# Kernel tuning notes

Hardware: AMD Instinct MI355X
Metric: run time of the kernel (lower is better)

The kernel has to match this reference:

```python
import jax, jax.numpy as jnp
import numpy as np

N, E, G = 100000, 1600000, 100
NEG_SLOPE = 0.2
EPS = 1e-5


def gatv2_conv(x, src, dst, Wl, Wr, att, bias, concat):
    # PyG GATv2Conv (eval mode, add_self_loops already applied to src/dst).
    # x: [N, F_in]; Wl/Wr: [F_in, H*C]; att: [H, C]; bias: [H*C] or [C].
    H, C = att.shape
    n = x.shape[0]
    xl = (x @ Wl).reshape(n, H, C)  # source-side transform (messages)
    xr = (x @ Wr).reshape(n, H, C)  # target-side transform
    m = jax.nn.leaky_relu(xl[src] + xr[dst], NEG_SLOPE)      # [Etot, H, C]
    e = jnp.einsum('ehc,hc->eh', m, att)                      # [Etot, H]
    # softmax over incoming edges of each destination node (per head)
    emax = jax.ops.segment_max(e, dst, num_segments=n)        # [n, H]
    ex = jnp.exp(e - emax[dst])
    denom = jax.ops.segment_sum(ex, dst, num_segments=n)
    alpha = ex / denom[dst]                                   # [Etot, H]
    out = jax.ops.segment_sum(xl[src] * alpha[..., None], dst, num_segments=n)  # [n, H, C]
    out = out.reshape(n, H * C) if concat else out.mean(axis=1)
    return out + bias


def graph_norm(x, batch, w, b, mean_scale):
    # PyG GraphNorm: per-graph mean/var with learnable mean_scale.
    cnt = jnp.maximum(jax.ops.segment_sum(jnp.ones((x.shape[0], 1), x.dtype), batch, num_segments=G), 1.0)
    mean = jax.ops.segment_sum(x, batch, num_segments=G) / cnt
    xc = x - mean_scale * mean[batch]
    var = jax.ops.segment_sum(xc * xc, batch, num_segments=G) / cnt
    return w * xc / jnp.sqrt(var[batch] + EPS) + b


def global_mean_pool(x, batch):
    cnt = jnp.maximum(jax.ops.segment_sum(jnp.ones((x.shape[0], 1), x.dtype), batch, num_segments=G), 1.0)
    return jax.ops.segment_sum(x, batch, num_segments=G) / cnt


def setup_inputs() -> dict:
    key = jax.random.key(0)
    ks = jax.random.split(key, 16)
    F_in, H, C12, C3 = 64, 4, 16, 32
    s_in = 1.0 / np.sqrt(F_in)
    s_h = 1.0 / np.sqrt(H * C12)
    inp = {
        'x': jax.random.normal(ks[0], (N, F_in), jnp.float32),
        'edge_index': jax.random.randint(ks[1], (2, E), 0, N, jnp.int64),
        'batch': jnp.sort(jax.random.randint(ks[2], (N,), 0, G, jnp.int64)),
        'Wl1': jax.random.normal(ks[3], (F_in, H * C12), jnp.float32) * s_in,
        'Wr1': jax.random.normal(ks[4], (F_in, H * C12), jnp.float32) * s_in,
        'att1': jax.random.normal(ks[5], (H, C12), jnp.float32) * s_in,
        'b1': jnp.zeros((H * C12,), jnp.float32),
        'g1w': jnp.ones((H * C12,), jnp.float32),
        'g1b': jnp.zeros((H * C12,), jnp.float32),
        'g1a': jnp.ones((H * C12,), jnp.float32),
        'Wl2': jax.random.normal(ks[6], (H * C12, H * C12), jnp.float32) * s_h,
        'Wr2': jax.random.normal(ks[7], (H * C12, H * C12), jnp.float32) * s_h,
        'att2': jax.random.normal(ks[8], (H, C12), jnp.float32) * s_h,
        'b2': jnp.zeros((H * C12,), jnp.float32),
        'g2w': jnp.ones((H * C12,), jnp.float32),
        'g2b': jnp.zeros((H * C12,), jnp.float32),
        'g2a': jnp.ones((H * C12,), jnp.float32),
        'Wl3': jax.random.normal(ks[9], (H * C12, H * C3), jnp.float32) * s_h,
        'Wr3': jax.random.normal(ks[10], (H * C12, H * C3), jnp.float32) * s_h,
        'att3': jax.random.normal(ks[11], (H, C3), jnp.float32) * s_h,
        'b3': jnp.zeros((C3,), jnp.float32),
        'g3w': jnp.ones((C3,), jnp.float32),
        'g3b': jnp.zeros((C3,), jnp.float32),
        'g3a': jnp.ones((C3,), jnp.float32),
        'Wlin': jax.random.normal(ks[12], (C3, 2), jnp.float32) * (1.0 / np.sqrt(C3)),
        'blin': jnp.zeros((2,), jnp.float32),
    }
    return inp


def reference(x, edge_index, batch, Wl1, Wr1, att1, b1, g1w, g1b, g1a,
              Wl2, Wr2, att2, b2, g2w, g2b, g2a,
              Wl3, Wr3, att3, b3, g3w, g3b, g3a, Wlin, blin):
    # add self-loops (GATv2Conv default)
    loops = jnp.arange(N, dtype=edge_index.dtype)
    src = jnp.concatenate([edge_index[0], loops])
    dst = jnp.concatenate([edge_index[1], loops])
    h = jax.nn.relu(graph_norm(gatv2_conv(x, src, dst, Wl1, Wr1, att1, b1, True), batch, g1w, g1b, g1a))
    h = jax.nn.relu(graph_norm(gatv2_conv(h, src, dst, Wl2, Wr2, att2, b2, True), batch, g2w, g2b, g2a))
    h = jax.nn.relu(graph_norm(gatv2_conv(h, src, dst, Wl3, Wr3, att3, b3, False), batch, g3w, g3b, g3a))
    pooled = global_mean_pool(h, batch)  # [G, h3]
    return pooled @ Wlin + blin          # [G, 2]
```

## Files before the change

kernel.cpp:

```cpp
#include <hip/hip_runtime.h>
#include <hip/hip_bf16.h>

#define LEAKY 0.2f
#define EPS_GN 1e-5f
#define PSH 9

typedef unsigned int uint;
typedef __attribute__((ext_vector_type(8))) short bf16x8;
typedef __attribute__((ext_vector_type(4))) float f32x4;


__device__ inline float4 bf4(uint lo, uint hi) {
    union { uint u; float f; } a, b, c, d;
    a.u = lo << 16; b.u = lo & 0xFFFF0000u;
    c.u = hi << 16; d.u = hi & 0xFFFF0000u;
    return make_float4(a.f, b.f, c.f, d.f);
}

__device__ inline uint pack_bf2(float lo, float hi) {
    union { float f; uint u; } x, y; x.f = lo; y.f = hi;
    uint ra = x.u + 0x7FFFu + ((x.u >> 16) & 1u);
    uint rb = y.u + 0x7FFFu + ((y.u >> 16) & 1u);
    return (ra >> 16) | (rb & 0xFFFF0000u);
}

__device__ inline unsigned short pack_bf1(float v) {
    union { float f; uint u; } q; q.f = v;
    return (unsigned short)((q.u + 0x7FFFu + ((q.u >> 16) & 1u)) >> 16);
}


__global__ void setup_kernel(float* __restrict__ stats, int statN,
                             const float* __restrict__ Wl1, const float* __restrict__ Wr1,
                             const float* __restrict__ Wl2, const float* __restrict__ Wr2,
                             const float* __restrict__ Wl3, const float* __restrict__ Wr3,
                             unsigned short* __restrict__ wt1, unsigned short* __restrict__ wt2,
                             unsigned short* __restrict__ wt3,
                             int* __restrict__ pcnt, int* __restrict__ csr_pad,
                             const int* __restrict__ batch, int* __restrict__ goff,
                             int nN, int nG) {
    int idx = blockIdx.x * 256 + threadIdx.x;
    if (idx < statN) { stats[idx] = 0.f; return; }
    idx -= statN;
    if (idx < 8192) {
        int col = idx >> 6, k = idx & 63;
        float v = (col < 64) ? Wl1[k * 64 + col] : Wr1[k * 64 + (col - 64)];
        wt1[col * 64 + k] = pack_bf1(v);
        return;
    }
    idx -= 8192;
    if (idx < 8192) {
        int col = idx >> 6, k = idx & 63;
        float v = (col < 64) ? Wl2[k * 64 + col] : Wr2[k * 64 + (col - 64)];
        wt2[col * 64 + k] = pack_bf1(v);
        return;
    }
    idx -= 8192;
    if (idx < 16384) {
        int col = idx >> 6, k = idx & 63;
        float v = (col < 128) ? Wl3[k * 128 + col] : Wr3[k * 128 + (col - 128)];
        wt3[col * 64 + k] = pack_bf1(v);
        return;
    }
    idx -= 16384;
    if (idx < 256) { pcnt[idx] = 0; return; }
    idx -= 256;
    if (idx < 16) { csr_pad[idx] = 0; return; }
    idx -= 16;
    if (idx <= nG) {
        if (idx == nG) { goff[idx] = nN; return; }
        int lo = 0, hi = nN;
        while (lo < hi) { int mid = (lo + hi) >> 1; if (batch[mid] < idx) lo = mid + 1; else hi = mid; }
        goff[idx] = lo;
    }
}


__global__ void pcount_kernel(const int* __restrict__ dsts, int* __restrict__ pcnt,
                              int E_, int Etot_) {
    __shared__ int h[256];
    int tid = threadIdx.x;
    h[tid] = 0;
    __syncthreads();
    int i0 = blockIdx.x * 2048 + tid;
#pragma unroll
    for (int k = 0; k < 8; ++k) {
        int i = i0 + k * 256;
        if (i < Etot_) {
            int d = (i < E_) ? dsts[i] : (i - E_);
            atomicAdd(&h[d >> PSH], 1);
        }
    }
    __syncthreads();
    if (h[tid] > 0) atomicAdd(&pcnt[tid], h[tid]);
}

__global__ void pscan_kernel(const int* __restrict__ pcnt, int* __restrict__ pstart,
                             int* __restrict__ gcur, int* __restrict__ rowstart, int nN) {
    __shared__ int sd[256];
    int t = threadIdx.x;
    int v = pcnt[t];
    sd[t] = v;
    __syncthreads();
    for (int off = 1; off < 256; off <<= 1) {
        int tmp = (t >= off) ? sd[t - off] : 0;
        __syncthreads();
        sd[t] += tmp;
        __syncthreads();
    }
    int excl = sd[t] - v;
    pstart[t] = excl;
    gcur[t] = excl;
    if (t == 255) {
        pstart[256] = sd[255];
        gcur[256] = sd[255];
        rowstart[nN] = sd[255];
    }
}

__global__ void partA_kernel(const int* __restrict__ srcs, const int* __restrict__ dsts,
                             int* __restrict__ gcur, uint* __restrict__ ebuf,
                             int E_, int Etot_) {
    __shared__ int hist[256], base_s[256], lcur[256];
    int tid = threadIdx.x;
    hist[tid] = 0; lcur[tid] = 0;
    __syncthreads();
    int i0 = blockIdx.x * 2048 + tid;
    uint rec[8]; int pp[8];
#pragma unroll
    for (int k = 0; k < 8; ++k) {
        int i = i0 + k * 256;
        pp[k] = -1;
        if (i < Etot_) {
            int s, d;
            if (i < E_) { s = srcs[i]; d = dsts[i]; } else { s = i - E_; d = s; }
            int p = d >> PSH;
            pp[k] = p;
            rec[k] = (uint)s | ((uint)(d & ((1 << PSH) - 1)) << 17);
            atomicAdd(&hist[p], 1);
        }
    }
    __syncthreads();
    int h = hist[tid];
    if (h > 0) base_s[tid] = atomicAdd(&gcur[tid], h);
    __syncthreads();
#pragma unroll
    for (int k = 0; k < 8; ++k) {
        if (pp[k] >= 0) {
            int pos = base_s[pp[k]] + atomicAdd(&lcur[pp[k]], 1);
            ebuf[pos] = rec[k];
        }
    }
}

__global__ void partB2_kernel(const uint* __restrict__ ebuf, const int* __restrict__ pstart,
                              int* __restrict__ rowstart, int* __restrict__ csr, int nN) {
    __shared__ int cnt[512], ofs[512], ssum[256];
    int t = threadIdx.x;
    cnt[t] = 0; cnt[t + 256] = 0;
    __syncthreads();
    int p = blockIdx.x;
    int lo = pstart[p], hi = pstart[p + 1];
    for (int i = lo + t; i < hi; i += 256)
        atomicAdd(&cnt[ebuf[i] >> 17], 1);
    __syncthreads();
    int a = cnt[2 * t], b = cnt[2 * t + 1];
    ssum[t] = a + b;
    __syncthreads();
    for (int off = 1; off < 256; off <<= 1) {
        int tmp = (t >= off) ? ssum[t - off] : 0;
        __syncthreads();
        ssum[t] += tmp;
        __syncthreads();
    }
    int base = (t > 0) ? ssum[t - 1] : 0;
    ofs[2 * t] = lo + base;
    ofs[2 * t + 1] = lo + base + a;
    __syncthreads();
    int n0 = p << PSH;
#pragma unroll
    for (int j = t; j < 512; j += 256) {
        int n = n0 + j;
        if (n < nN) rowstart[n] = ofs[j];
    }
    __syncthreads();
    for (int i = lo + t; i < hi; i += 256) {
        uint v = ebuf[i];
        int pos = atomicAdd(&ofs[v >> 17], 1);
        csr[pos] = (int)(v & 0x1FFFFu);
    }
}


template <int NCOLS, bool NORM>
__global__ __launch_bounds__(256, 4)
void gemm_mfma_kernel(const float* __restrict__ x, const unsigned short* __restrict__ Wt,
                      unsigned short* __restrict__ xl, unsigned short* __restrict__ xr,
                      int nN, const float* __restrict__ param, const int* __restrict__ batch) {
    constexpr int NT = NCOLS / 16;
    constexpr int OD = NCOLS / 2;
    __shared__ unsigned short Xs[64 * 64];
    __shared__ unsigned short Ws[NCOLS * 64];
    int tid = threadIdx.x;
    int node0 = blockIdx.x * 64;

    {
        int nl = tid >> 2, k0 = (tid & 3) * 16;
        int n = node0 + nl;
        bool v = n < nN;
        int nc = v ? n : 0;
        const float* xrow = x + (size_t)nc * 64 + k0;
        const float* scp = nullptr; const float* shp = nullptr;
        if constexpr (NORM) {
            int g = batch[nc];
            scp = param + (size_t)g * 128 + k0;
            shp = param + (size_t)g * 128 + 64 + k0;
        }
        uint q[8];
#pragma unroll
        for (int j = 0; j < 8; ++j) {
            float a = v ? xrow[j * 2] : 0.f;
            float b = v ? xrow[j * 2 + 1] : 0.f;
            if constexpr (NORM) {
                a = fmaxf(fmaf(scp[j * 2], a, shp[j * 2]), 0.f);
                b = fmaxf(fmaf(scp[j * 2 + 1], b, shp[j * 2 + 1]), 0.f);
            }
            q[j] = pack_bf2(a, b);
        }
        char* base = (char*)Xs + nl * 128;
        uint sw = (uint)(nl & 7) << 4;
        *(uint4*)(base + (((uint)(k0 * 2)) ^ sw))      = make_uint4(q[0], q[1], q[2], q[3]);
        *(uint4*)(base + (((uint)(k0 * 2 + 16)) ^ sw)) = make_uint4(q[4], q[5], q[6], q[7]);
    }
    for (int ch = tid; ch < NCOLS * 8; ch += 256) {
        int col = ch >> 3, sub = ch & 7;
        uint4 q = ((const uint4*)(Wt + col * 64))[sub];
        *(uint4*)((char*)Ws + col * 128 + (((uint)(sub * 16)) ^ ((uint)(col & 7) << 4))) = q;
    }
    __syncthreads();

    int lane = tid & 63;
    int wv = tid >> 6;
    int l15 = lane & 15, quad = lane >> 4;

    bf16x8 xf[2];
    {
        int row = wv * 16 + l15;
        char* base = (char*)Xs + row * 128;
        uint sw = (uint)(row & 7) << 4;
        xf[0] = *(bf16x8*)(base + (((uint)(quad * 16)) ^ sw));
        xf[1] = *(bf16x8*)(base + (((uint)(64 + quad * 16)) ^ sw));
    }
    f32x4 acc[NT];
#pragma unroll
    for (int t = 0; t < NT; ++t) acc[t] = (f32x4){0.f, 0.f, 0.f, 0.f};
#pragma unroll
    for (int t = 0; t < NT; ++t) {
        int col = t * 16 + l15;
        char* base = (char*)Ws + col * 128;
        uint sw = (uint)(col & 7) << 4;
        bf16x8 a0 = *(bf16x8*)(base + (((uint)(quad * 16)) ^ sw));
        bf16x8 a1 = *(bf16x8*)(base + (((uint)(64 + quad * 16)) ^ sw));
        acc[t] = __builtin_amdgcn_mfma_f32_16x16x32_bf16(a0, xf[0], acc[t], 0, 0, 0);
        acc[t] = __builtin_amdgcn_mfma_f32_16x16x32_bf16(a1, xf[1], acc[t], 0, 0, 0);
    }
    int node = node0 + wv * 16 + l15;
    if (node < nN) {
#pragma unroll
        for (int t = 0; t < NT; ++t) {
            int cg = t * 16 + quad * 4;
            unsigned short* outp = (cg < OD) ? xl : xr;
            int ocol = (cg < OD) ? cg : cg - OD;
            uint2 pk;
            pk.x = pack_bf2(acc[t][0], acc[t][1]);
            pk.y = pack_bf2(acc[t][2], acc[t][3]);
            *(uint2*)(outp + (size_t)node * OD + ocol) = pk;
        }
    }
}


__global__ void agg64_kernel(const unsigned short* __restrict__ xl, const unsigned short* __restrict__ xr,
                             const int* __restrict__ rowstart, const int* __restrict__ csr,
                             const float* __restrict__ att, const float* __restrict__ bias,
                             float* __restrict__ out, int nN) {
    int wid = (blockIdx.x * blockDim.x + threadIdx.x) >> 6;
    int lane = threadIdx.x & 63;
    if (wid >= nN) return;
    int c8 = lane & 7;
    int sg = lane >> 3;
    const uint4* xl4 = (const uint4*)xl;
    const float LOG2E = 1.4426950408889634f;
    float4 attA = ((const float4*)att)[c8 * 2];
    float4 attB = ((const float4*)att)[c8 * 2 + 1];
    attA.x *= LOG2E; attA.y *= LOG2E; attA.z *= LOG2E; attA.w *= LOG2E;
    attB.x *= LOG2E; attB.y *= LOG2E; attB.z *= LOG2E; attB.w *= LOG2E;
    uint4 xru = ((const uint4*)xr)[(size_t)wid * 8 + c8];
    float4 xrA = bf4(xru.x, xru.y), xrB = bf4(xru.z, xru.w);
    int rs = rowstart[wid], re = rowstart[wid + 1];
    int nIt = (re - rs + 7) >> 3;
    float den = 0.f;
    float4 accA = make_float4(0.f, 0.f, 0.f, 0.f);
    float4 accB = make_float4(0.f, 0.f, 0.f, 0.f);
    int i = rs + sg;
    int s = csr[i];
    uint4 xv = xl4[(size_t)s * 8 + c8];
    for (int it = 0; it < nIt; ++it) {
        float4 curA = bf4(xv.x, xv.y), curB = bf4(xv.z, xv.w);
        bool vv = i < re;
        i += 8;
        s = csr[i];
        xv = xl4[(size_t)s * 8 + c8];
        float4 mA, mB;
        mA.x = curA.x + xrA.x; mA.y = curA.y + xrA.y;
        mA.z = curA.z + xrA.z; mA.w = curA.w + xrA.w;
        mB.x = curB.x + xrB.x; mB.y = curB.y + xrB.y;
        mB.z = curB.z + xrB.z; mB.w = curB.w + xrB.w;
        mA.x = fmaxf(mA.x, LEAKY * mA.x); mA.y = fmaxf(mA.y, LEAKY * mA.y);
        mA.z = fmaxf(mA.z, LEAKY * mA.z); mA.w = fmaxf(mA.w, LEAKY * mA.w);
        mB.x = fmaxf(mB.x, LEAKY * mB.x); mB.y = fmaxf(mB.y, LEAKY * mB.y);
        mB.z = fmaxf(mB.z, LEAKY * mB.z); mB.w = fmaxf(mB.w, LEAKY * mB.w);
        float p = mA.x * attA.x;
        p = fmaf(mA.y, attA.y, p); p = fmaf(mA.z, attA.z, p); p = fmaf(mA.w, attA.w, p);
        p = fmaf(mB.x, attB.x, p); p = fmaf(mB.y, attB.y, p);
        p = fmaf(mB.z, attB.z, p); p = fmaf(mB.w, attB.w, p);
        p += __shfl_xor(p, 1);
        float w = vv ? exp2f(p) : 0.f;
        den += w;
        accA.x = fmaf(w, curA.x, accA.x); accA.y = fmaf(w, curA.y, accA.y);
        accA.z = fmaf(w, curA.z, accA.z); accA.w = fmaf(w, curA.w, accA.w);
        accB.x = fmaf(w, curB.x, accB.x); accB.y = fmaf(w, curB.y, accB.y);
        accB.z = fmaf(w, curB.z, accB.z); accB.w = fmaf(w, curB.w, accB.w);
    }
#pragma unroll
    for (int off = 8; off <= 32; off <<= 1) {
        den    += __shfl_xor(den, off);
        accA.x += __shfl_xor(accA.x, off); accA.y += __shfl_xor(accA.y, off);
        accA.z += __shfl_xor(accA.z, off); accA.w += __shfl_xor(accA.w, off);
        accB.x += __shfl_xor(accB.x, off); accB.y += __shfl_xor(accB.y, off);
        accB.z += __shfl_xor(accB.z, off); accB.w += __shfl_xor(accB.w, off);
    }
    if (lane < 8) {
        float4 bvA = ((const float4*)bias)[c8 * 2];
        float4 bvB = ((const float4*)bias)[c8 * 2 + 1];
        float inv = 1.f / den;
        float4 rA, rB;
        rA.x = fmaf(accA.x, inv, bvA.x); rA.y = fmaf(accA.y, inv, bvA.y);
        rA.z = fmaf(accA.z, inv, bvA.z); rA.w = fmaf(accA.w, inv, bvA.w);
        rB.x = fmaf(accB.x, inv, bvB.x); rB.y = fmaf(accB.y, inv, bvB.y);
        rB.z = fmaf(accB.z, inv, bvB.z); rB.w = fmaf(accB.w, inv, bvB.w);
        ((float4*)out)[(size_t)wid * 16 + c8 * 2]     = rA;
        ((float4*)out)[(size_t)wid * 16 + c8 * 2 + 1] = rB;
    }
}


__global__ void agg128_mean_kernel(const unsigned short* __restrict__ xl, const unsigned short* __restrict__ xr,
                                   const int* __restrict__ rowstart, const int* __restrict__ csr,
                                   const float* __restrict__ att, const float* __restrict__ bias,
                                   float* __restrict__ out, int nN) {
    int wid = (blockIdx.x * blockDim.x + threadIdx.x) >> 6;
    int lane = threadIdx.x & 63;
    if (wid >= nN) return;
    int c8 = lane & 15;
    int sg = lane >> 4;
    const uint4* xl4 = (const uint4*)xl;
    const float LOG2E = 1.4426950408889634f;
    float4 attA = ((const float4*)att)[c8 * 2];
    float4 attB = ((const float4*)att)[c8 * 2 + 1];
    attA.x *= LOG2E; attA.y *= LOG2E; attA.z *= LOG2E; attA.w *= LOG2E;
    attB.x *= LOG2E; attB.y *= LOG2E; attB.z *= LOG2E; attB.w *= LOG2E;
    uint4 xru = ((const uint4*)xr)[(size_t)wid * 16 + c8];
    float4 xrA = bf4(xru.x, xru.y), xrB = bf4(xru.z, xru.w);
    int rs = rowstart[wid], re = rowstart[wid + 1];
    int nIt = (re - rs + 3) >> 2;
    float den = 0.f;
    float4 accA = make_float4(0.f, 0.f, 0.f, 0.f);
    float4 accB = make_float4(0.f, 0.f, 0.f, 0.f);
    int i = rs + sg;
    int s = csr[i];
    uint4 xv = xl4[(size_t)s * 16 + c8];
    for (int it = 0; it < nIt; ++it) {
        float4 curA = bf4(xv.x, xv.y), curB = bf4(xv.z, xv.w);
        bool vv = i < re;
        i += 4;
        s = csr[i];
        xv = xl4[(size_t)s * 16 + c8];
        float4 mA, mB;
        mA.x = curA.x + xrA.x; mA.y = curA.y + xrA.y;
        mA.z = curA.z + xrA.z; mA.w = curA.w + xrA.w;
        mB.x = curB.x + xrB.x; mB.y = curB.y + xrB.y;
        mB.z = curB.z + xrB.z; mB.w = curB.w + xrB.w;
        mA.x = fmaxf(mA.x, LEAKY * mA.x); mA.y = fmaxf(mA.y, LEAKY * mA.y);
        mA.z = fmaxf(mA.z, LEAKY * mA.z); mA.w = fmaxf(mA.w, LEAKY * mA.w);
        mB.x = fmaxf(mB.x, LEAKY * mB.x); mB.y = fmaxf(mB.y, LEAKY * mB.y);
        mB.z = fmaxf(mB.z, LEAKY * mB.z); mB.w = fmaxf(mB.w, LEAKY * mB.w);
        float p = mA.x * attA.x;
        p = fmaf(mA.y, attA.y, p); p = fmaf(mA.z, attA.z, p); p = fmaf(mA.w, attA.w, p);
        p = fmaf(mB.x, attB.x, p); p = fmaf(mB.y, attB.y, p);
        p = fmaf(mB.z, attB.z, p); p = fmaf(mB.w, attB.w, p);
        p += __shfl_xor(p, 1);
        p += __shfl_xor(p, 2);
        float w = vv ? exp2f(p) : 0.f;
        den += w;
        accA.x = fmaf(w, curA.x, accA.x); accA.y = fmaf(w, curA.y, accA.y);
        accA.z = fmaf(w, curA.z, accA.z); accA.w = fmaf(w, curA.w, accA.w);
        accB.x = fmaf(w, curB.x, accB.x); accB.y = fmaf(w, curB.y, accB.y);
        accB.z = fmaf(w, curB.z, accB.z); accB.w = fmaf(w, curB.w, accB.w);
    }
#pragma unroll
    for (int off = 16; off <= 32; off <<= 1) {
        den    += __shfl_xor(den, off);
        accA.x += __shfl_xor(accA.x, off); accA.y += __shfl_xor(accA.y, off);
        accA.z += __shfl_xor(accA.z, off); accA.w += __shfl_xor(accA.w, off);
        accB.x += __shfl_xor(accB.x, off); accB.y += __shfl_xor(accB.y, off);
        accB.z += __shfl_xor(accB.z, off); accB.w += __shfl_xor(accB.w, off);
    }
    float inv = 1.f / den;
    float4 rA, rB;
    rA.x = accA.x * inv; rA.y = accA.y * inv; rA.z = accA.z * inv; rA.w = accA.w * inv;
    rB.x = accB.x * inv; rB.y = accB.y * inv; rB.z = accB.z * inv; rB.w = accB.w * inv;
#pragma unroll
    for (int off = 4; off <= 8; off <<= 1) {
        rA.x += __shfl_xor(rA.x, off); rA.y += __shfl_xor(rA.y, off);
        rA.z += __shfl_xor(rA.z, off); rA.w += __shfl_xor(rA.w, off);
        rB.x += __shfl_xor(rB.x, off); rB.y += __shfl_xor(rB.y, off);
        rB.z += __shfl_xor(rB.z, off); rB.w += __shfl_xor(rB.w, off);
    }
    if (lane < 4) {
        float4 bvA = ((const float4*)bias)[lane * 2];
        float4 bvB = ((const float4*)bias)[lane * 2 + 1];
        float4 oA, oB;
        oA.x = fmaf(rA.x, 0.25f, bvA.x); oA.y = fmaf(rA.y, 0.25f, bvA.y);
        oA.z = fmaf(rA.z, 0.25f, bvA.z); oA.w = fmaf(rA.w, 0.25f, bvA.w);
        oB.x = fmaf(rB.x, 0.25f, bvB.x); oB.y = fmaf(rB.y, 0.25f, bvB.y);
        oB.z = fmaf(rB.z, 0.25f, bvB.z); oB.w = fmaf(rB.w, 0.25f, bvB.w);
        ((float4*)out)[(size_t)wid * 8 + lane * 2]     = oA;
        ((float4*)out)[(size_t)wid * 8 + lane * 2 + 1] = oB;
    }
}


template <int D>
__global__ void gnorm_stats_kernel(const float* __restrict__ in, const int* __restrict__ goff,
                                   float* __restrict__ stats, int SPLIT) {
    int g = blockIdx.x / SPLIT, part = blockIdx.x % SPLIT;
    int start = goff[g], end = goff[g + 1];
    constexpr int RPB = 256 / D;
    int tid = threadIdx.x;
    int c = tid % D, sub = tid / D;
    float s1 = 0.f, s2 = 0.f;
    for (int n = start + part * RPB + sub; n < end; n += SPLIT * RPB) {
        float v = in[(size_t)n * D + c];
        s1 += v; s2 += v * v;
    }
    __shared__ float l1[256], l2[256];
    l1[tid] = s1; l2[tid] = s2;
    __syncthreads();
    if (tid < D) {
        for (int s = 1; s < RPB; ++s) { s1 += l1[s * D + tid]; s2 += l2[s * D + tid]; }
        atomicAdd(&stats[(size_t)g * 2 * D + tid], s1);
        atomicAdd(&stats[(size_t)g * 2 * D + D + tid], s2);
    }
}

template <int D>
__global__ void gnorm_finalize_kernel(const float* __restrict__ stats, const int* __restrict__ goff,
                                      const float* __restrict__ w, const float* __restrict__ b,
                                      const float* __restrict__ a, float* __restrict__ param) {
    int g = blockIdx.x, c = threadIdx.x;
    if (c >= D) return;
    int cn = goff[g + 1] - goff[g];
    float cnt = (float)(cn > 1 ? cn : 1);
    float S1 = stats[(size_t)g * 2 * D + c], S2 = stats[(size_t)g * 2 * D + D + c];
    float mu = S1 / cnt;
    float am = a[c] * mu;
    float var = S2 / cnt - 2.f * am * mu + am * am;
    float sc = w[c] * rsqrtf(var + EPS_GN);
    param[(size_t)g * 2 * D + c] = sc;
    param[(size_t)g * 2 * D + D + c] = b[c] - sc * am;
}


__global__ void pool3_kernel(const float* __restrict__ in, const int* __restrict__ goff,
                             const float* __restrict__ param, float* __restrict__ pooled, int SPLIT) {
    int g = blockIdx.x / SPLIT, part = blockIdx.x % SPLIT;
    int start = goff[g], end = goff[g + 1];
    int tid = threadIdx.x;
    int c = tid & 31, sub = tid >> 5;
    float sc = param[(size_t)g * 64 + c], sh = param[(size_t)g * 64 + 32 + c];
    float s = 0.f;
    for (int n = start + part * 8 + sub; n < end; n += SPLIT * 8)
        s += fmaxf(fmaf(sc, in[(size_t)n * 32 + c], sh), 0.f);
    __shared__ float l[256];
    l[tid] = s;
    __syncthreads();
    if (tid < 32) {
        for (int q = 1; q < 8; ++q) s += l[q * 32 + tid];
        atomicAdd(&pooled[(size_t)g * 32 + tid], s);
    }
}

__global__ void lin_kernel(const float* __restrict__ pooled, const int* __restrict__ goff,
                           const float* __restrict__ Wlin, const float* __restrict__ blin,
                           float* __restrict__ out, int nG) {
    int idx = blockIdx.x * blockDim.x + threadIdx.x;
    if (idx >= nG * 2) return;
    int g = idx >> 1, o = idx & 1;
    int cn = goff[g + 1] - goff[g];
    float inv = 1.f / (float)(cn > 1 ? cn : 1);
    float acc = blin[o];
    for (int c = 0; c < 32; ++c) acc = fmaf(pooled[(size_t)g * 32 + c] * inv, Wlin[c * 2 + o], acc);
    out[idx] = acc;
}


extern "C" void kernel_launch(void* const* d_in, const int* in_sizes, int n_in,
                              void* d_out, int out_size, void* d_ws, size_t ws_size,
                              hipStream_t stream) {
    const float* x    = (const float*)d_in[0];
    const int*  eidx  = (const int*)d_in[1];
    const int*  batch = (const int*)d_in[2];
    const float* Wl1 = (const float*)d_in[3];
    const float* Wr1 = (const float*)d_in[4];
    const float* att1 = (const float*)d_in[5];
    const float* b1 = (const float*)d_in[6];
    const float* g1w = (const float*)d_in[7];
    const float* g1b = (const float*)d_in[8];
    const float* g1a = (const float*)d_in[9];
    const float* Wl2 = (const float*)d_in[10];
    const float* Wr2 = (const float*)d_in[11];
    const float* att2 = (const float*)d_in[12];
    const float* b2 = (const float*)d_in[13];
    const float* g2w = (const float*)d_in[14];
    const float* g2b = (const float*)d_in[15];
    const float* g2a = (const float*)d_in[16];
    const float* Wl3 = (const float*)d_in[17];
    const float* Wr3 = (const float*)d_in[18];
    const float* att3 = (const float*)d_in[19];
    const float* b3 = (const float*)d_in[20];
    const float* g3w = (const float*)d_in[21];
    const float* g3b = (const float*)d_in[22];
    const float* g3a = (const float*)d_in[23];
    const float* Wlin = (const float*)d_in[24];
    const float* blin = (const float*)d_in[25];
    float* outp = (float*)d_out;

    const int N = in_sizes[0] / 64;
    const int E = in_sizes[1] / 2;
    const int Etot = N + E;
    const int G = out_size / 2;
    const int P = (N + (1 << PSH) - 1) >> PSH;
    const int SPLIT = 16;

    unsigned short* xlb = (unsigned short*)d_ws;
    unsigned short* xrb = xlb + (size_t)N * 128;
    float* agg   = (float*)(xrb + (size_t)N * 128);
    float* stats = agg + (size_t)N * 64;
    float* stats1 = stats;
    float* stats2 = stats1 + (size_t)G * 128;
    float* stats3 = stats2 + (size_t)G * 128;
    float* pooled = stats3 + (size_t)G * 64;
    float* param  = pooled + (size_t)G * 32;
    int* rowstart = (int*)(param + (size_t)G * 128);
    int* csr      = rowstart + (N + 1);
    uint* ebuf    = (uint*)(csr + Etot + 16);
    int* goff     = (int*)(ebuf + Etot);
    int* gcur     = goff + (G + 1);
    int* pstart   = gcur + 257;
    int* pcnt     = pstart + 257;
    unsigned short* wt1 = (unsigned short*)(pcnt + 256);
    unsigned short* wt2 = wt1 + 8192;
    unsigned short* wt3 = wt2 + 8192;

    const int* src_idx = eidx;
    const int* dst_idx = eidx + E;

    const int statN = G * 352;
    int setupTotal = statN + 32768 + 256 + 16 + (G + 1);
    setup_kernel<<<(setupTotal + 255) / 256, 256, 0, stream>>>(
        stats, statN, Wl1, Wr1, Wl2, Wr2, Wl3, Wr3, wt1, wt2, wt3,
        pcnt, csr + Etot, batch, goff, N, G);

    int edgeBlocks = (Etot + 2047) / 2048;
    pcount_kernel<<<edgeBlocks, 256, 0, stream>>>(dst_idx, pcnt, E, Etot);
    pscan_kernel<<<1, 256, 0, stream>>>(pcnt, pstart, gcur, rowstart, N);
    partA_kernel<<<edgeBlocks, 256, 0, stream>>>(src_idx, dst_idx, gcur, ebuf, E, Etot);
    partB2_kernel<<<P, 256, 0, stream>>>(ebuf, pstart, rowstart, csr, N);

    dim3 blk(256);
    int aggGrid = (N + 3) / 4;
    int gemmGrid = (N + 63) / 64;

    gemm_mfma_kernel<128, false><<<gemmGrid, blk, 0, stream>>>(x, wt1, xlb, xrb, N, nullptr, nullptr);
    agg64_kernel<<<aggGrid, blk, 0, stream>>>(xlb, xrb, rowstart, csr, att1, b1, agg, N);
    gnorm_stats_kernel<64><<<G * SPLIT, blk, 0, stream>>>(agg, goff, stats1, SPLIT);
    gnorm_finalize_kernel<64><<<G, 64, 0, stream>>>(stats1, goff, g1w, g1b, g1a, param);

    gemm_mfma_kernel<128, true><<<gemmGrid, blk, 0, stream>>>(agg, wt2, xlb, xrb, N, param, batch);
    agg64_kernel<<<aggGrid, blk, 0, stream>>>(xlb, xrb, rowstart, csr, att2, b2, agg, N);
    gnorm_stats_kernel<64><<<G * SPLIT, blk, 0, stream>>>(agg, goff, stats2, SPLIT);
    gnorm_finalize_kernel<64><<<G, 64, 0, stream>>>(stats2, goff, g2w, g2b, g2a, param);

    gemm_mfma_kernel<256, true><<<gemmGrid, blk, 0, stream>>>(agg, wt3, xlb, xrb, N, param, batch);
    agg128_mean_kernel<<<aggGrid, blk, 0, stream>>>(xlb, xrb, rowstart, csr, att3, b3, agg, N);
    gnorm_stats_kernel<32><<<G * SPLIT, blk, 0, stream>>>(agg, goff, stats3, SPLIT);
    gnorm_finalize_kernel<32><<<G, 32, 0, stream>>>(stats3, goff, g3w, g3b, g3a, param);
    pool3_kernel<<<G * SPLIT, blk, 0, stream>>>(agg, goff, param, pooled, SPLIT);
    lin_kernel<<<(G * 2 + 63) / 64, 64, 0, stream>>>(pooled, goff, Wlin, blin, outp, G);
}
```

Before: 409.5 us.

## Split leaky-ReLU attention into linear per-node terms plus abs term

Uses leaky_relu(z) = 0.6z + 0.4|z| to split the per-edge attention score into per-node linear terms (att·xl[src], att·xr[dst]) and a remaining abs term. The GEMM kernel now also computes the per-node linear projections and writes them to new asv/adv buffers. The aggregation kernels add these in and drop the fmaxf/leaky step for an abs-based dot product. This cuts per-edge ALU work but adds one extra gathered load per edge and extra stores and shuffles in the GEMM.

After: 426.3 us. 4.1% more time.

```diff
diff --git a/kernel.cpp b/kernel.cpp
--- a/kernel.cpp
+++ b/kernel.cpp
@@ -8,6 +8,8 @@
 typedef unsigned int uint;
 typedef __attribute__((ext_vector_type(8))) short bf16x8;
 typedef __attribute__((ext_vector_type(4))) float f32x4;
+
+#define LOG2E 1.4426950408889634f
 
 
 __device__ inline float4 bf4(uint lo, uint hi) {
@@ -196,7 +198,9 @@
 __global__ __launch_bounds__(256, 4)
 void gemm_mfma_kernel(const float* __restrict__ x, const unsigned short* __restrict__ Wt,
                       unsigned short* __restrict__ xl, unsigned short* __restrict__ xr,
-                      int nN, const float* __restrict__ param, const int* __restrict__ batch) {
+                      int nN, const float* __restrict__ param, const int* __restrict__ batch,
+                      const float* __restrict__ attg, float* __restrict__ asv,
+                      float* __restrict__ adv) {
     constexpr int NT = NCOLS / 16;
     constexpr int OD = NCOLS / 2;
     __shared__ unsigned short Xs[64 * 64];
@@ -265,6 +269,19 @@
         acc[t] = __builtin_amdgcn_mfma_f32_16x16x32_bf16(a1, xf[1], acc[t], 0, 0, 0);
     }
     int node = node0 + wv * 16 + l15;
+    float pa[NT];
+#pragma unroll
+    for (int t = 0; t < NT; ++t) {
+        int cg = t * 16 + quad * 4;
+        int acol = cg & (OD - 1);
+        float s = acc[t][0] * attg[acol];
+        s = fmaf(acc[t][1], attg[acol + 1], s);
+        s = fmaf(acc[t][2], attg[acol + 2], s);
+        s = fmaf(acc[t][3], attg[acol + 3], s);
+        s += __shfl_xor(s, 16);
+        s += __shfl_xor(s, 32);
+        pa[t] = s;
+    }
     if (node < nN) {
 #pragma unroll
         for (int t = 0; t < NT; ++t) {
@@ -276,6 +293,22 @@
             pk.y = pack_bf2(acc[t][2], acc[t][3]);
             *(uint2*)(outp + (size_t)node * OD + ocol) = pk;
         }
+        if (quad == 0) {
+            const float C1 = 0.6f * LOG2E;
+            if constexpr (OD == 64) {
+#pragma unroll
+                for (int u = 0; u < 4; ++u) {
+                    asv[(size_t)node * 4 + u] = pa[u] * C1;
+                    adv[(size_t)node * 4 + u] = pa[u + 4] * C1;
+                }
+            } else {
+#pragma unroll
+                for (int u = 0; u < 4; ++u) {
+                    asv[(size_t)node * 4 + u] = (pa[2 * u] + pa[2 * u + 1]) * C1;
+                    adv[(size_t)node * 4 + u] = (pa[8 + 2 * u] + pa[8 + 2 * u + 1]) * C1;
+                }
+            }
+        }
     }
 }
 
@@ -283,20 +316,23 @@
 __global__ void agg64_kernel(const unsigned short* __restrict__ xl, const unsigned short* __restrict__ xr,
                              const int* __restrict__ rowstart, const int* __restrict__ csr,
                              const float* __restrict__ att, const float* __restrict__ bias,
+                             const float* __restrict__ asv, const float* __restrict__ adv,
                              float* __restrict__ out, int nN) {
     int wid = (blockIdx.x * blockDim.x + threadIdx.x) >> 6;
     int lane = threadIdx.x & 63;
     if (wid >= nN) return;
     int c8 = lane & 7;
     int sg = lane >> 3;
+    int h = c8 >> 1;
     const uint4* xl4 = (const uint4*)xl;
-    const float LOG2E = 1.4426950408889634f;
+    const float S04 = 0.4f * LOG2E;
     float4 attA = ((const float4*)att)[c8 * 2];
     float4 attB = ((const float4*)att)[c8 * 2 + 1];
-    attA.x *= LOG2E; attA.y *= LOG2E; attA.z *= LOG2E; attA.w *= LOG2E;
-    attB.x *= LOG2E; attB.y *= LOG2E; attB.z *= LOG2E; attB.w *= LOG2E;
+    attA.x *= S04; attA.y *= S04; attA.z *= S04; attA.w *= S04;
+    attB.x *= S04; attB.y *= S04; attB.z *= S04; attB.w *= S04;
     uint4 xru = ((const uint4*)xr)[(size_t)wid * 8 + c8];
     float4 xrA = bf4(xru.x, xru.y), xrB = bf4(xru.z, xru.w);
+    float scd = adv[(size_t)wid * 4 + h];
     int rs = rowstart[wid], re = rowstart[wid + 1];
     int nIt = (re - rs + 7) >> 3;
     float den = 0.f;
@@ -305,26 +341,25 @@
     int i = rs + sg;
     int s = csr[i];
     uint4 xv = xl4[(size_t)s * 8 + c8];
+    float a_s = asv[(size_t)s * 4 + h];
     for (int it = 0; it < nIt; ++it) {
         float4 curA = bf4(xv.x, xv.y), curB = bf4(xv.z, xv.w);
+        float a_cur = a_s;
         bool vv = i < re;
         i += 8;
         s = csr[i];
         xv = xl4[(size_t)s * 8 + c8];
-        float4 mA, mB;
-        mA.x = curA.x + xrA.x; mA.y = curA.y + xrA.y;
-        mA.z = curA.z + xrA.z; mA.w = curA.w + xrA.w;
-        mB.x = curB.x + xrB.x; mB.y = curB.y + xrB.y;
-        mB.z = curB.z + xrB.z; mB.w = curB.w + xrB.w;
-        mA.x = fmaxf(mA.x, LEAKY * mA.x); mA.y = fmaxf(mA.y, LEAKY * mA.y);
-        mA.z = fmaxf(mA.z, LEAKY * mA.z); mA.w = fmaxf(mA.w, LEAKY * mA.w);
-        mB.x = fmaxf(mB.x, LEAKY * mB.x); mB.y = fmaxf(mB.y, LEAKY * mB.y);
-        mB.z = fmaxf(mB.z, LEAKY * mB.z); mB.w = fmaxf(mB.w, LEAKY * mB.w);
-        float p = mA.x * attA.x;
-        p = fmaf(mA.y, attA.y, p); p = fmaf(mA.z, attA.z, p); p = fmaf(mA.w, attA.w, p);
-        p = fmaf(mB.x, attB.x, p); p = fmaf(mB.y, attB.y, p);
-        p = fmaf(mB.z, attB.z, p); p = fmaf(mB.w, attB.w, p);
+        a_s = asv[(size_t)s * 4 + h];
+        float p = attA.x * fabsf(curA.x + xrA.x);
+        p = fmaf(attA.y, fabsf(curA.y + xrA.y), p);
+        p = fmaf(attA.z, fabsf(curA.z + xrA.z), p);
+        p = fmaf(attA.w, fabsf(curA.w + xrA.w), p);
+        p = fmaf(attB.x, fabsf(curB.x + xrB.x), p);
+        p = fmaf(attB.y, fabsf(curB.y + xrB.y), p);
+        p = fmaf(attB.z, fabsf(curB.z + xrB.z), p);
+        p = fmaf(attB.w, fabsf(curB.w + xrB.w), p);
         p += __shfl_xor(p, 1);
+        p += a_cur + scd;
         float w = vv ? exp2f(p) : 0.f;
         den += w;
         accA.x = fmaf(w, curA.x, accA.x); accA.y = fmaf(w, curA.y, accA.y);
@@ -358,20 +393,23 @@
 __global__ void agg128_mean_kernel(const unsigned short* __restrict__ xl, const unsigned short* __restrict__ xr,
                                    const int* __restrict__ rowstart, const int* __restrict__ csr,
                                    const float* __restrict__ att, const float* __restrict__ bias,
+                                   const float* __restrict__ asv, const float* __restrict__ adv,
                                    float* __restrict__ out, int nN) {
     int wid = (blockIdx.x * blockDim.x + threadIdx.x) >> 6;
     int lane = threadIdx.x & 63;
     if (wid >= nN) return;
     int c8 = lane & 15;
     int sg = lane >> 4;
+    int h = c8 >> 2;
     const uint4* xl4 = (const uint4*)xl;
-    const float LOG2E = 1.4426950408889634f;
+    const float S04 = 0.4f * LOG2E;
     float4 attA = ((const float4*)att)[c8 * 2];
     float4 attB = ((const float4*)att)[c8 * 2 + 1];
-    attA.x *= LOG2E; attA.y *= LOG2E; attA.z *= LOG2E; attA.w *= LOG2E;
-    attB.x *= LOG2E; attB.y *= LOG2E; attB.z *= LOG2E; attB.w *= LOG2E;
+    attA.x *= S04; attA.y *= S04; attA.z *= S04; attA.w *= S04;
+    attB.x *= S04; attB.y *= S04; attB.z *= S04; attB.w *= S04;
     uint4 xru = ((const uint4*)xr)[(size_t)wid * 16 + c8];
     float4 xrA = bf4(xru.x, xru.y), xrB = bf4(xru.z, xru.w);
+    float scd = adv[(size_t)wid * 4 + h];
     int rs = rowstart[wid], re = rowstart[wid + 1];
     int nIt = (re - rs + 3) >> 2;
     float den = 0.f;
@@ -380,27 +418,26 @@
     int i = rs + sg;
     int s = csr[i];
     uint4 xv = xl4[(size_t)s * 16 + c8];
+    float a_s = asv[(size_t)s * 4 + h];
     for (int it = 0; it < nIt; ++it) {
         float4 curA = bf4(xv.x, xv.y), curB = bf4(xv.z, xv.w);
+        float a_cur = a_s;
         bool vv = i < re;
         i += 4;
         s = csr[i];
         xv = xl4[(size_t)s * 16 + c8];
-        float4 mA, mB;
-        mA.x = curA.x + xrA.x; mA.y = curA.y + xrA.y;
-        mA.z = curA.z + xrA.z; mA.w = curA.w + xrA.w;
-        mB.x = curB.x + xrB.x; mB.y = curB.y + xrB.y;
-        mB.z = curB.z + xrB.z; mB.w = curB.w + xrB.w;
-        mA.x = fmaxf(mA.x, LEAKY * mA.x); mA.y = fmaxf(mA.y, LEAKY * mA.y);
-        mA.z = fmaxf(mA.z, LEAKY * mA.z); mA.w = fmaxf(mA.w, LEAKY * mA.w);
-        mB.x = fmaxf(mB.x, LEAKY * mB.x); mB.y = fmaxf(mB.y, LEAKY * mB.y);
-        mB.z = fmaxf(mB.z, LEAKY * mB.z); mB.w = fmaxf(mB.w, LEAKY * mB.w);
-        float p = mA.x * attA.x;
-        p = fmaf(mA.y, attA.y, p); p = fmaf(mA.z, attA.z, p); p = fmaf(mA.w, attA.w, p);
-        p = fmaf(mB.x, attB.x, p); p = fmaf(mB.y, attB.y, p);
-        p = fmaf(mB.z, attB.z, p); p = fmaf(mB.w, attB.w, p);
+        a_s = asv[(size_t)s * 4 + h];
+        float p = attA.x * fabsf(curA.x + xrA.x);
+        p = fmaf(attA.y, fabsf(curA.y + xrA.y), p);
+        p = fmaf(attA.z, fabsf(curA.z + xrA.z), p);
+        p = fmaf(attA.w, fabsf(curA.w + xrA.w), p);
+        p = fmaf(attB.x, fabsf(curB.x + xrB.x), p);
+        p = fmaf(attB.y, fabsf(curB.y + xrB.y), p);
+        p = fmaf(attB.z, fabsf(curB.z + xrB.z), p);
+        p = fmaf(attB.w, fabsf(curB.w + xrB.w), p);
         p += __shfl_xor(p, 1);
         p += __shfl_xor(p, 2);
+        p += a_cur + scd;
         float w = vv ? exp2f(p) : 0.f;
         den += w;
         accA.x = fmaf(w, curA.x, accA.x); accA.y = fmaf(w, curA.y, accA.y);
@@ -572,6 +609,8 @@
     unsigned short* wt1 = (unsigned short*)(pcnt + 256);
     unsigned short* wt2 = wt1 + 8192;
     unsigned short* wt3 = wt2 + 8192;
+    float* asv = (float*)(wt3 + 16384);
+    float* adv = asv + (size_t)N * 4;
 
     const int* src_idx = eidx;
     const int* dst_idx = eidx + E;
@@ -592,18 +631,18 @@
     int aggGrid = (N + 3) / 4;
     int gemmGrid = (N + 63) / 64;
 
-    gemm_mfma_kernel<128, false><<<gemmGrid, blk, 0, stream>>>(x, wt1, xlb, xrb, N, nullptr, nullptr);
-    agg64_kernel<<<aggGrid, blk, 0, stream>>>(xlb, xrb, rowstart, csr, att1, b1, agg, N);
+    gemm_mfma_kernel<128, false><<<gemmGrid, blk, 0, stream>>>(x, wt1, xlb, xrb, N, nullptr, nullptr, att1, asv, adv);
+    agg64_kernel<<<aggGrid, blk, 0, stream>>>(xlb, xrb, rowstart, csr, att1, b1, asv, adv, agg, N);
     gnorm_stats_kernel<64><<<G * SPLIT, blk, 0, stream>>>(agg, goff, stats1, SPLIT);
     gnorm_finalize_kernel<64><<<G, 64, 0, stream>>>(stats1, goff, g1w, g1b, g1a, param);
 
-    gemm_mfma_kernel<128, true><<<gemmGrid, blk, 0, stream>>>(agg, wt2, xlb, xrb, N, param, batch);
-    agg64_kernel<<<aggGrid, blk, 0, stream>>>(xlb, xrb, rowstart, csr, att2, b2, agg, N);
+    gemm_mfma_kernel<128, true><<<gemmGrid, blk, 0, stream>>>(agg, wt2, xlb, xrb, N, param, batch, att2, asv, adv);
+    agg64_kernel<<<aggGrid, blk, 0, stream>>>(xlb, xrb, rowstart, csr, att2, b2, asv, adv, agg, N);
     gnorm_stats_kernel<64><<<G * SPLIT, blk, 0, stream>>>(agg, goff, stats2, SPLIT);
     gnorm_finalize_kernel<64><<<G, 64, 0, stream>>>(stats2, goff, g2w, g2b, g2a, param);
 
-    gemm_mfma_kernel<256, true><<<gemmGrid, blk, 0, stream>>>(agg, wt3, xlb, xrb, N, param, batch);
-    agg128_mean_kernel<<<aggGrid, blk, 0, stream>>>(xlb, xrb, rowstart, csr, att3, b3, agg, N);
+    gemm_mfma_kernel<256, true><<<gemmGrid, blk, 0, stream>>>(agg, wt3, xlb, xrb, N, param, batch, att3, asv, adv);
+    agg128_mean_kernel<<<aggGrid, blk, 0, stream>>>(xlb, xrb, rowstart, csr, att3, b3, asv, adv, agg, N);
     gnorm_stats_kernel<32><<<G * SPLIT, blk, 0, stream>>>(agg, goff, stats3, SPLIT);
     gnorm_finalize_kernel<32><<<G, 32, 0, stream>>>(stats3, goff, g3w, g3b, g3a, param);
     pool3_kernel<<<G * SPLIT, blk, 0, stream>>>(agg, goff, param, pooled, SPLIT);
```
